# Kernel tuning notes

Measured on AMD Instinct MI355X. Metric: run time of the kernel, lower is better.

## Reference

```python
import jax, jax.numpy as jnp
import numpy as np

HEADS = 8
DIM_HEAD = 64


def setup_inputs() -> dict:
    key = jax.random.key(0)
    ks = jax.random.split(key, 4)
    B, C, H, W = 1, 256, 64, 64
    inner = HEADS * DIM_HEAD  # 512
    x = jax.random.normal(ks[0], (B, C, H, W), dtype=jnp.float32)
    norm_w = jnp.ones((C,), dtype=jnp.float32)                      # RMSNorm weight (1,C,1,1) flattened
    w_qkv = jax.random.normal(ks[1], (3 * inner, C), dtype=jnp.float32) * 0.02  # 1x1 conv, no bias
    w_out = jax.random.normal(ks[2], (C, inner), dtype=jnp.float32) * 0.02      # 1x1 conv
    b_out = jax.random.normal(ks[3], (C,), dtype=jnp.float32) * 0.02
    return {"x": x, "norm_w": norm_w, "w_qkv": w_qkv, "w_out": w_out, "b_out": b_out}


def reference(x, norm_w, w_qkv, w_out, b_out):
    B, C, H, W = x.shape
    N = H * W
    # RMSNorm: F.normalize over channel dim (L2, eps clamp) * weight * sqrt(C)
    l2 = jnp.sqrt(jnp.sum(x * x, axis=1, keepdims=True))
    xn = x / jnp.maximum(l2, 1e-12) * norm_w[None, :, None, None] * (C ** 0.5)
    # 1x1 conv QKV = channel matmul
    qkv = jnp.einsum('oc,bchw->bohw', w_qkv, xn)  # [B, 3*inner, H, W]
    q, k, v = jnp.split(qkv, 3, axis=1)

    def split_heads(t):
        # 'b (h d) x y -> b h (x y) d'
        return t.reshape(B, HEADS, DIM_HEAD, N).transpose(0, 1, 3, 2)

    q, k, v = map(split_heads, (q, k, v))
    scale = DIM_HEAD ** -0.5
    scores = jnp.einsum('bhnd,bhmd->bhnm', q, k) * scale  # [B,H,N,N]
    attn = jax.nn.softmax(scores, axis=-1)
    out = jnp.einsum('bhnm,bhmd->bhnd', attn, v)
    # 'b h (x y) d -> b (h d) x y'
    out = out.transpose(0, 1, 3, 2).reshape(B, HEADS * DIM_HEAD, H, W)
    # output 1x1 conv + residual (note: residual is the NORMALIZED x, per source)
    return jnp.einsum('ci,bihw->bchw', w_out, out) + b_out[None, :, None, None] + xn
```

## Files before the change

kernel.cpp:

```cpp
#include <hip/hip_runtime.h>


#define NPIX 4096
#define CIN 256
#define INNER 512
#define NHEAD 8
#define DH 64

typedef _Float16 f16;
typedef __attribute__((ext_vector_type(8))) _Float16 f16x8;
typedef __attribute__((ext_vector_type(4))) float f32x4;

static __device__ __forceinline__ f32x4 mfma_f16(f16x8 a, f16x8 b, f32x4 c) {
  return __builtin_amdgcn_mfma_f32_16x16x32_f16(a, b, c, 0, 0, 0);
}

static __device__ __forceinline__ unsigned pk2(float lo, float hi) {
  return __builtin_bit_cast(unsigned, __builtin_amdgcn_cvt_pkrtz(lo, hi));
}

static __device__ __forceinline__ float unpk_lo(unsigned u) {
  return (float)__builtin_bit_cast(f16, (unsigned short)(u & 0xffffu));
}
static __device__ __forceinline__ float unpk_hi(unsigned u) {
  return (float)__builtin_bit_cast(f16, (unsigned short)(u >> 16));
}

__global__ __launch_bounds__(256) void k_cvt2(const float* __restrict__ a,
                                              f16* __restrict__ b, int na,
                                              const float* __restrict__ c,
                                              f16* __restrict__ d, int nc) {
  int i = (blockIdx.x * 256 + threadIdx.x) * 2;
  if (i < na) {
    float2 v = *(const float2*)(a + i);
    ((unsigned*)b)[i >> 1] = pk2(v.x, v.y);
  } else {
    int j = i - na;
    if (j < nc) {
      float2 v = *(const float2*)(c + j);
      ((unsigned*)d)[j >> 1] = pk2(v.x, v.y);
    }
  }
}

__global__ __launch_bounds__(256) void k_rmsnorm(const float* __restrict__ x,
                                                 const float* __restrict__ w,
                                                 float* __restrict__ xn,
                                                 f16* __restrict__ xnT) {
  const int pi = threadIdx.x & 15, cs = threadIdx.x >> 4;
  const int p = blockIdx.x * 16 + pi;
  __shared__ float red[16][16];
  float ss = 0.f;
  for (int i = 0; i < 16; ++i) {
    float v = x[(cs * 16 + i) * NPIX + p];
    ss += v * v;
  }
  red[cs][pi] = ss;
  __syncthreads();
  float tot = 0.f;
#pragma unroll
  for (int s = 0; s < 16; ++s) tot += red[s][pi];
  float inv = 16.0f / fmaxf(sqrtf(tot), 1e-12f);
  for (int i = 0; i < 16; ++i) {
    int c = cs * 16 + i;
    float v = x[c * NPIX + p] * inv * w[c];
    xn[c * NPIX + p] = v;
    xnT[p * CIN + c] = (f16)v;
  }
}

__global__ __launch_bounds__(256) void k_qkv(const f16* __restrict__ wqkv,
                                             const f16* __restrict__ xnT,
                                             f16* __restrict__ qT,
                                             f16* __restrict__ kT,
                                             f16* __restrict__ vv) {
  const int lane = threadIdx.x & 63, wave = threadIdx.x >> 6;
  const int l15 = lane & 15, quad = lane >> 4;
  const int obase = blockIdx.y * 64 + (wave >> 1) * 32;
  const int pbase = blockIdx.x * 128 + (wave & 1) * 64;
  const int sect = blockIdx.y >> 3;
  f32x4 acc[8];
#pragma unroll
  for (int i = 0; i < 8; ++i) acc[i] = (f32x4){0.f, 0.f, 0.f, 0.f};
#pragma unroll
  for (int kc = 0; kc < CIN / 32; ++kc) {
    f16x8 af[2], bfr[4];
#pragma unroll
    for (int oc = 0; oc < 2; ++oc)
      af[oc] = *(const f16x8*)(wqkv + (size_t)(obase + oc * 16 + l15) * CIN + kc * 32 + quad * 8);
#pragma unroll
    for (int pc = 0; pc < 4; ++pc)
      bfr[pc] = *(const f16x8*)(xnT + (size_t)(pbase + pc * 16 + l15) * CIN + kc * 32 + quad * 8);
    if (sect < 2) {
#pragma unroll
      for (int pc = 0; pc < 4; ++pc)
#pragma unroll
        for (int oc = 0; oc < 2; ++oc)
          acc[pc * 2 + oc] = mfma_f16(bfr[pc], af[oc], acc[pc * 2 + oc]);
    } else {
#pragma unroll
      for (int oc = 0; oc < 2; ++oc)
#pragma unroll
        for (int pc = 0; pc < 4; ++pc)
          acc[oc * 4 + pc] = mfma_f16(af[oc], bfr[pc], acc[oc * 4 + pc]);
    }
  }
  if (sect < 2) {
    f16* dst = (sect == 0) ? qT : kT;
    const float sc = (sect == 0) ? 0.18033688f : 1.0f;
    const int head = blockIdx.y & 7;
    const int dd = (wave >> 1) * 32;
#pragma unroll
    for (int pc = 0; pc < 4; ++pc)
#pragma unroll
      for (int oc = 0; oc < 2; ++oc)
#pragma unroll
        for (int r = 0; r < 4; ++r) {
          int p = pbase + pc * 16 + quad * 4 + r;
          dst[((size_t)(head << 12) + p) * DH + dd + oc * 16 + l15] =
              (f16)(acc[pc * 2 + oc][r] * sc);
        }
  } else {
#pragma unroll
    for (int oc = 0; oc < 2; ++oc)
#pragma unroll
      for (int r = 0; r < 4; ++r) {
        int o = obase + oc * 16 + quad * 4 + r - 2 * INNER;
#pragma unroll
        for (int pc = 0; pc < 4; ++pc)
          vv[(size_t)o * NPIX + pbase + pc * 16 + l15] = (f16)acc[oc * 4 + pc][r];
      }
  }
}

__global__ __launch_bounds__(256, 2) void k_attn(const f16* __restrict__ qT,
                                                 const f16* __restrict__ kT,
                                                 const f16* __restrict__ vv,
                                                 f16* __restrict__ Ows) {
  const int head = blockIdx.x & 7;
  const int qb = (blockIdx.x >> 3) * 64;
  const int tid = threadIdx.x;
  const int wave = tid >> 6, lane = tid & 63;
  const int l15 = lane & 15, quad = lane >> 4;

  __shared__ unsigned Omp[4][4][16][33];
  __shared__ float Ll[4][4][16];

  f16x8 qf[4][2];
#pragma unroll
  for (int qt = 0; qt < 4; ++qt)
#pragma unroll
    for (int kc = 0; kc < 2; ++kc)
      qf[qt][kc] = *(const f16x8*)(qT + ((size_t)(head << 12) + qb + qt * 16 + l15) * DH + kc * 32 + quad * 8);

  f32x4 o[4][4], ol[4];
#pragma unroll
  for (int qt = 0; qt < 4; ++qt) {
#pragma unroll
    for (int c = 0; c < 4; ++c) o[qt][c] = (f32x4){0.f, 0.f, 0.f, 0.f};
    ol[qt] = (f32x4){0.f, 0.f, 0.f, 0.f};
  }

  const f16* kbase = kT + (size_t)(head << 12) * DH;
  const f16* vbase = vv + (size_t)(head * DH) * NPIX;
  const int kb0 = wave * (NPIX / 4);
  const int srcA = ((quad & 1) << 5) + l15;
  const int srcB = srcA + 16;
  const bool hiQuad = quad >= 2;
  const f16x8 onesv = {1.f16, 1.f16, 1.f16, 1.f16, 1.f16, 1.f16, 1.f16, 1.f16};

  f16x8 kf[2][2], kfn[2][2];
#pragma unroll
  for (int nc = 0; nc < 2; ++nc)
#pragma unroll
    for (int kc = 0; kc < 2; ++kc)
      kf[nc][kc] = *(const f16x8*)(kbase + (size_t)(kb0 + nc * 16 + l15) * DH + kc * 32 + quad * 8);

  for (int it = 0; it < 32; ++it) {
    const int kb = kb0 + it * 32;
    f16x8 vf[4];
#pragma unroll
    for (int c = 0; c < 4; ++c)
      vf[c] = *(const f16x8*)(vbase + (size_t)(c * 16 + l15) * NPIX + kb + quad * 8);
    const int kbn = kb0 + ((it + 1) & 31) * 32;
#pragma unroll
    for (int nc = 0; nc < 2; ++nc)
#pragma unroll
      for (int kc = 0; kc < 2; ++kc)
        kfn[nc][kc] = *(const f16x8*)(kbase + (size_t)(kbn + nc * 16 + l15) * DH + kc * 32 + quad * 8);

    f32x4 s[4][2];
#pragma unroll
    for (int qt = 0; qt < 4; ++qt)
#pragma unroll
      for (int nc = 0; nc < 2; ++nc) {
        s[qt][nc] = mfma_f16(kf[nc][0], qf[qt][0], (f32x4){0.f, 0.f, 0.f, 0.f});
        s[qt][nc] = mfma_f16(kf[nc][1], qf[qt][1], s[qt][nc]);
      }

#pragma unroll
    for (int qt = 0; qt < 4; ++qt) {
      float p0[4], p1[4];
#pragma unroll
      for (int r = 0; r < 4; ++r) {
        p0[r] = __builtin_amdgcn_exp2f(s[qt][0][r]);
        p1[r] = __builtin_amdgcn_exp2f(s[qt][1][r]);
      }
      unsigned A0 = pk2(p0[0], p0[1]), B0 = pk2(p0[2], p0[3]);
      unsigned A1 = pk2(p1[0], p1[1]), B1 = pk2(p1[2], p1[3]);
      unsigned As = hiQuad ? A1 : A0;
      unsigned Bs = hiQuad ? B1 : B0;
      union { f16x8 v; unsigned u[4]; } pf;
      pf.u[0] = (unsigned)__shfl((int)As, srcA);
      pf.u[1] = (unsigned)__shfl((int)Bs, srcA);
      pf.u[2] = (unsigned)__shfl((int)As, srcB);
      pf.u[3] = (unsigned)__shfl((int)Bs, srcB);
#pragma unroll
      for (int c = 0; c < 4; ++c) o[qt][c] = mfma_f16(vf[c], pf.v, o[qt][c]);
      ol[qt] = mfma_f16(onesv, pf.v, ol[qt]);
    }

#pragma unroll
    for (int nc = 0; nc < 2; ++nc)
#pragma unroll
      for (int kc = 0; kc < 2; ++kc) kf[nc][kc] = kfn[nc][kc];
  }

#pragma unroll
  for (int qt = 0; qt < 4; ++qt) {
    if (quad == 0) Ll[wave][qt][l15] = ol[qt][0];
#pragma unroll
    for (int c = 0; c < 4; ++c) {
      Omp[wave][qt][l15][c * 8 + quad * 2] = pk2(o[qt][c][0], o[qt][c][1]);
      Omp[wave][qt][l15][c * 8 + quad * 2 + 1] = pk2(o[qt][c][2], o[qt][c][3]);
    }
  }
  __syncthreads();

  const int dp = tid & 31;
  const int q0 = tid >> 5;
  unsigned* OwsU = (unsigned*)Ows;
#pragma unroll
  for (int qt = 0; qt < 4; ++qt)
#pragma unroll
    for (int h = 0; h < 2; ++h) {
      int q = q0 + h * 8;
      float a = 0.f, b = 0.f, L = 0.f;
#pragma unroll
      for (int w = 0; w < 4; ++w) {
        unsigned u = Omp[w][qt][q][dp];
        a += unpk_lo(u);
        b += unpk_hi(u);
        L += Ll[w][qt][q];
      }
      float rL = 1.0f / L;
      OwsU[((size_t)(head << 12) + qb + qt * 16 + q) * (DH / 2) + dp] =
          pk2(a * rL, b * rL);
    }
}

__global__ __launch_bounds__(256) void k_oproj(const f16* __restrict__ wout,
                                               const f16* __restrict__ Ows,
                                               const float* __restrict__ bout,
                                               const float* __restrict__ xn,
                                               float* __restrict__ out) {
  const int lane = threadIdx.x & 63, wave = threadIdx.x >> 6;
  const int l15 = lane & 15, quad = lane >> 4;
  const int mbase = blockIdx.y * 32 + (wave >> 1) * 16;
  const int pbase = blockIdx.x * 64 + (wave & 1) * 32;
  f32x4 acc[2];
  acc[0] = (f32x4){0.f, 0.f, 0.f, 0.f};
  acc[1] = (f32x4){0.f, 0.f, 0.f, 0.f};
#pragma unroll
  for (int kc = 0; kc < INNER / 32; ++kc) {
    f16x8 af = *(const f16x8*)(wout + (size_t)(mbase + l15) * INNER + kc * 32 + quad * 8);
    int i0 = kc * 32 + quad * 8;
    int head = i0 >> 6, d0 = i0 & 63;
#pragma unroll
    for (int pc = 0; pc < 2; ++pc) {
      f16x8 bfr = *(const f16x8*)(Ows + ((size_t)(head << 12) + pbase + pc * 16 + l15) * DH + d0);
      acc[pc] = mfma_f16(af, bfr, acc[pc]);
    }
  }
#pragma unroll
  for (int pc = 0; pc < 2; ++pc)
#pragma unroll
    for (int r = 0; r < 4; ++r) {
      int c = mbase + quad * 4 + r, p = pbase + pc * 16 + l15;
      out[c * NPIX + p] = acc[pc][r] + bout[c] + xn[c * NPIX + p];
    }
}

extern "C" void kernel_launch(void* const* d_in, const int* in_sizes, int n_in,
                              void* d_out, int out_size, void* d_ws, size_t ws_size,
                              hipStream_t stream) {
  (void)in_sizes; (void)n_in; (void)out_size; (void)ws_size;
  const float* x      = (const float*)d_in[0];
  const float* norm_w = (const float*)d_in[1];
  const float* w_qkv  = (const float*)d_in[2];
  const float* w_out  = (const float*)d_in[3];
  const float* b_out  = (const float*)d_in[4];
  float* out = (float*)d_out;

  char* ws = (char*)d_ws;
  float* xn    = (float*)(ws);
  f16* xnT     = (f16*)(ws + (4u << 20));
  f16* qT      = (f16*)(ws + (6u << 20));
  f16* kT      = (f16*)(ws + (10u << 20));
  f16* vv      = (f16*)(ws + (14u << 20));
  f16* Ows     = (f16*)(ws + (18u << 20));
  f16* wqkv_h  = (f16*)(ws + (22u << 20));
  f16* wout_h  = (f16*)(ws + (23u << 20));

  const int na = 3 * INNER * CIN, nc = CIN * INNER;
  hipLaunchKernelGGL(k_cvt2, dim3((na + nc) / 512), dim3(256), 0, stream,
                     w_qkv, wqkv_h, na, w_out, wout_h, nc);
  hipLaunchKernelGGL(k_rmsnorm, dim3(NPIX / 16), dim3(256), 0, stream, x, norm_w, xn, xnT);
  hipLaunchKernelGGL(k_qkv, dim3(NPIX / 128, 1536 / 64), dim3(256), 0, stream,
                     wqkv_h, xnT, qT, kT, vv);
  hipLaunchKernelGGL(k_attn, dim3(512), dim3(256), 0, stream, qT, kT, vv, Ows);
  hipLaunchKernelGGL(k_oproj, dim3(NPIX / 64, CIN / 32), dim3(256), 0, stream,
                     wout_h, Ows, b_out, xn, out);
}
```

Baseline: 169.9 us.

## Fuse weight conversion into GEMMs, vectorize RMSNorm stores, halve attention query tile

Drops the separate weight fp32→fp16 conversion kernel. The QKV and output-projection GEMMs now load fp32 weights and convert them in registers, which saves one launch and a round trip through the workspace, but the weights are re-read at double width by every block. RMSNorm keeps x in registers instead of reading it twice and writes the transposed fp16 output as packed 16-byte stores. The attention kernel processes 32 queries per block instead of 64 over 1024 blocks, which raises parallelism but means each block streams the full K/V for half as much work.

Measured after the change: 228.2 us. 1.34x slower.

```diff
diff --git a/kernel.cpp b/kernel.cpp
--- a/kernel.cpp
+++ b/kernel.cpp
@@ -26,21 +26,15 @@
   return (float)__builtin_bit_cast(f16, (unsigned short)(u >> 16));
 }
 
-__global__ __launch_bounds__(256) void k_cvt2(const float* __restrict__ a,
-                                              f16* __restrict__ b, int na,
-                                              const float* __restrict__ c,
-                                              f16* __restrict__ d, int nc) {
-  int i = (blockIdx.x * 256 + threadIdx.x) * 2;
-  if (i < na) {
-    float2 v = *(const float2*)(a + i);
-    ((unsigned*)b)[i >> 1] = pk2(v.x, v.y);
-  } else {
-    int j = i - na;
-    if (j < nc) {
-      float2 v = *(const float2*)(c + j);
-      ((unsigned*)d)[j >> 1] = pk2(v.x, v.y);
-    }
-  }
+static __device__ __forceinline__ f16x8 ld_cvt8(const float* __restrict__ p) {
+  float4 a = *(const float4*)p;
+  float4 b = *(const float4*)(p + 4);
+  union { f16x8 v; unsigned u[4]; } r;
+  r.u[0] = pk2(a.x, a.y);
+  r.u[1] = pk2(a.z, a.w);
+  r.u[2] = pk2(b.x, b.y);
+  r.u[3] = pk2(b.z, b.w);
+  return r.v;
 }
 
 __global__ __launch_bounds__(256) void k_rmsnorm(const float* __restrict__ x,
@@ -50,10 +44,12 @@
   const int pi = threadIdx.x & 15, cs = threadIdx.x >> 4;
   const int p = blockIdx.x * 16 + pi;
   __shared__ float red[16][16];
+  float v[16];
   float ss = 0.f;
+#pragma unroll
   for (int i = 0; i < 16; ++i) {
-    float v = x[(cs * 16 + i) * NPIX + p];
-    ss += v * v;
+    v[i] = x[(cs * 16 + i) * NPIX + p];
+    ss += v[i] * v[i];
   }
   red[cs][pi] = ss;
   __syncthreads();
@@ -61,15 +57,21 @@
 #pragma unroll
   for (int s = 0; s < 16; ++s) tot += red[s][pi];
   float inv = 16.0f / fmaxf(sqrtf(tot), 1e-12f);
+  union { unsigned u[8]; uint4 q[2]; } pkd;
+#pragma unroll
   for (int i = 0; i < 16; ++i) {
     int c = cs * 16 + i;
-    float v = x[c * NPIX + p] * inv * w[c];
-    xn[c * NPIX + p] = v;
-    xnT[p * CIN + c] = (f16)v;
-  }
-}
-
-__global__ __launch_bounds__(256) void k_qkv(const f16* __restrict__ wqkv,
+    v[i] = v[i] * inv * w[c];
+    xn[c * NPIX + p] = v[i];
+  }
+#pragma unroll
+  for (int j = 0; j < 8; ++j) pkd.u[j] = pk2(v[2 * j], v[2 * j + 1]);
+  uint4* dst = (uint4*)(xnT + (size_t)p * CIN + cs * 16);
+  dst[0] = pkd.q[0];
+  dst[1] = pkd.q[1];
+}
+
+__global__ __launch_bounds__(256) void k_qkv(const float* __restrict__ wqkv,
                                              const f16* __restrict__ xnT,
                                              f16* __restrict__ qT,
                                              f16* __restrict__ kT,
@@ -87,7 +89,7 @@
     f16x8 af[2], bfr[4];
 #pragma unroll
     for (int oc = 0; oc < 2; ++oc)
-      af[oc] = *(const f16x8*)(wqkv + (size_t)(obase + oc * 16 + l15) * CIN + kc * 32 + quad * 8);
+      af[oc] = ld_cvt8(wqkv + (size_t)(obase + oc * 16 + l15) * CIN + kc * 32 + quad * 8);
 #pragma unroll
     for (int pc = 0; pc < 4; ++pc)
       bfr[pc] = *(const f16x8*)(xnT + (size_t)(pbase + pc * 16 + l15) * CIN + kc * 32 + quad * 8);
@@ -138,24 +140,24 @@
                                                  const f16* __restrict__ vv,
                                                  f16* __restrict__ Ows) {
   const int head = blockIdx.x & 7;
-  const int qb = (blockIdx.x >> 3) * 64;
+  const int qb = (blockIdx.x >> 3) * 32;
   const int tid = threadIdx.x;
   const int wave = tid >> 6, lane = tid & 63;
   const int l15 = lane & 15, quad = lane >> 4;
 
-  __shared__ unsigned Omp[4][4][16][33];
-  __shared__ float Ll[4][4][16];
-
-  f16x8 qf[4][2];
-#pragma unroll
-  for (int qt = 0; qt < 4; ++qt)
+  __shared__ unsigned Omp[4][2][16][33];
+  __shared__ float Ll[4][2][16];
+
+  f16x8 qf[2][2];
+#pragma unroll
+  for (int qt = 0; qt < 2; ++qt)
 #pragma unroll
     for (int kc = 0; kc < 2; ++kc)
       qf[qt][kc] = *(const f16x8*)(qT + ((size_t)(head << 12) + qb + qt * 16 + l15) * DH + kc * 32 + quad * 8);
 
-  f32x4 o[4][4], ol[4];
-#pragma unroll
-  for (int qt = 0; qt < 4; ++qt) {
+  f32x4 o[2][4], ol[2];
+#pragma unroll
+  for (int qt = 0; qt < 2; ++qt) {
 #pragma unroll
     for (int c = 0; c < 4; ++c) o[qt][c] = (f32x4){0.f, 0.f, 0.f, 0.f};
     ol[qt] = (f32x4){0.f, 0.f, 0.f, 0.f};
@@ -189,9 +191,9 @@
       for (int kc = 0; kc < 2; ++kc)
         kfn[nc][kc] = *(const f16x8*)(kbase + (size_t)(kbn + nc * 16 + l15) * DH + kc * 32 + quad * 8);
 
-    f32x4 s[4][2];
-#pragma unroll
-    for (int qt = 0; qt < 4; ++qt)
+    f32x4 s[2][2];
+#pragma unroll
+    for (int qt = 0; qt < 2; ++qt)
 #pragma unroll
       for (int nc = 0; nc < 2; ++nc) {
         s[qt][nc] = mfma_f16(kf[nc][0], qf[qt][0], (f32x4){0.f, 0.f, 0.f, 0.f});
@@ -199,7 +201,7 @@
       }
 
 #pragma unroll
-    for (int qt = 0; qt < 4; ++qt) {
+    for (int qt = 0; qt < 2; ++qt) {
       float p0[4], p1[4];
 #pragma unroll
       for (int r = 0; r < 4; ++r) {
@@ -227,7 +229,7 @@
   }
 
 #pragma unroll
-  for (int qt = 0; qt < 4; ++qt) {
+  for (int qt = 0; qt < 2; ++qt) {
     if (quad == 0) Ll[wave][qt][l15] = ol[qt][0];
 #pragma unroll
     for (int c = 0; c < 4; ++c) {
@@ -241,7 +243,7 @@
   const int q0 = tid >> 5;
   unsigned* OwsU = (unsigned*)Ows;
 #pragma unroll
-  for (int qt = 0; qt < 4; ++qt)
+  for (int qt = 0; qt < 2; ++qt)
 #pragma unroll
     for (int h = 0; h < 2; ++h) {
       int q = q0 + h * 8;
@@ -259,7 +261,7 @@
     }
 }
 
-__global__ __launch_bounds__(256) void k_oproj(const f16* __restrict__ wout,
+__global__ __launch_bounds__(256) void k_oproj(const float* __restrict__ wout,
                                                const f16* __restrict__ Ows,
                                                const float* __restrict__ bout,
                                                const float* __restrict__ xn,
@@ -273,7 +275,7 @@
   acc[1] = (f32x4){0.f, 0.f, 0.f, 0.f};
 #pragma unroll
   for (int kc = 0; kc < INNER / 32; ++kc) {
-    f16x8 af = *(const f16x8*)(wout + (size_t)(mbase + l15) * INNER + kc * 32 + quad * 8);
+    f16x8 af = ld_cvt8(wout + (size_t)(mbase + l15) * INNER + kc * 32 + quad * 8);
     int i0 = kc * 32 + quad * 8;
     int head = i0 >> 6, d0 = i0 & 63;
 #pragma unroll
@@ -309,16 +311,11 @@
   f16* kT      = (f16*)(ws + (10u << 20));
   f16* vv      = (f16*)(ws + (14u << 20));
   f16* Ows     = (f16*)(ws + (18u << 20));
-  f16* wqkv_h  = (f16*)(ws + (22u << 20));
-  f16* wout_h  = (f16*)(ws + (23u << 20));
-
-  const int na = 3 * INNER * CIN, nc = CIN * INNER;
-  hipLaunchKernelGGL(k_cvt2, dim3((na + nc) / 512), dim3(256), 0, stream,
-                     w_qkv, wqkv_h, na, w_out, wout_h, nc);
+
   hipLaunchKernelGGL(k_rmsnorm, dim3(NPIX / 16), dim3(256), 0, stream, x, norm_w, xn, xnT);
   hipLaunchKernelGGL(k_qkv, dim3(NPIX / 128, 1536 / 64), dim3(256), 0, stream,
-                     wqkv_h, xnT, qT, kT, vv);
-  hipLaunchKernelGGL(k_attn, dim3(512), dim3(256), 0, stream, qT, kT, vv, Ows);
+                     w_qkv, xnT, qT, kT, vv);
+  hipLaunchKernelGGL(k_attn, dim3(1024), dim3(256), 0, stream, qT, kT, vv, Ows);
   hipLaunchKernelGGL(k_oproj, dim3(NPIX / 64, CIN / 32), dim3(256), 0, stream,
-                     wout_h, Ows, b_out, xn, out);
-}
+                     w_out, Ows, b_out, xn, out);
+}
```
